# Kernel tuning notes

Hardware: AMD Instinct MI355X
Metric: run time of the kernel (lower is better)

Reference implementation:

```python
import jax, jax.numpy as jnp
import numpy as np

N, E = 50000, 800000
F_IN, H, OUT, L = 32, 128, 20, 4


def setup_inputs() -> dict:
    key = jax.random.key(0)
    ks = jax.random.split(key, 32)
    s = 0.05  # weight scale
    inp = {
        "h": jax.random.normal(ks[0], (N, F_IN), jnp.float32),
        "x": jax.random.normal(ks[1], (N, 3), jnp.float32),
        "edges": jax.random.randint(ks[2], (2, E), 0, N, jnp.int32),
        # embeddings
        "emb_in_w": jax.random.normal(ks[3], (F_IN, H)) * s,
        "emb_in_b": jnp.zeros((H,)),
        "emb_out_w": jax.random.normal(ks[4], (H, H)) * s,
        "emb_out_b": jnp.zeros((H,)),
        # per-layer stacked params
        "edge_w1": jax.random.normal(ks[5], (L, 2 * H + 1, H)) * s,
        "edge_b1": jnp.zeros((L, H)),
        "edge_w2": jax.random.normal(ks[6], (L, H, H)) * s,
        "edge_b2": jnp.zeros((L, H)),
        "att_w": jax.random.normal(ks[7], (L, H, 1)) * s,
        "att_b": jnp.zeros((L, 1)),
        "coord_w1": jax.random.normal(ks[8], (L, H, H)) * s,
        "coord_b1": jnp.zeros((L, H)),
        "coord_w2": jax.random.normal(ks[9], (L, H, 1)) * s,  # no bias (egnn_clean)
        "node_w1": jax.random.normal(ks[10], (L, 2 * H, H)) * s,
        "node_b1": jnp.zeros((L, H)),
        "node_w2": jax.random.normal(ks[11], (L, H, H)) * s,
        "node_b2": jnp.zeros((L, H)),
        # head MLP
        "head_w1": jax.random.normal(ks[12], (H, H)) * s,
        "head_b1": jnp.zeros((H,)),
        "head_w2": jax.random.normal(ks[13], (H, OUT)) * s,
        "head_b2": jnp.zeros((OUT,)),
    }
    return inp


def reference(h, x, edges, emb_in_w, emb_in_b, emb_out_w, emb_out_b,
              edge_w1, edge_b1, edge_w2, edge_b2, att_w, att_b,
              coord_w1, coord_b1, coord_w2,
              node_w1, node_b1, node_w2, node_b2,
              head_w1, head_b1, head_w2, head_b2):
    n = h.shape[0]
    row, col = edges[0], edges[1]
    h = h @ emb_in_w + emb_in_b
    for l in range(L):
        diff = x[row] - x[col]                       # [E,3]
        radial = jnp.sum(diff * diff, -1, keepdims=True)  # [E,1]
        m = jnp.concatenate([h[row], h[col], radial], -1)  # [E,2H+1]
        m = jax.nn.silu(m @ edge_w1[l] + edge_b1[l])
        m = jax.nn.silu(m @ edge_w2[l] + edge_b2[l])
        m = m * jax.nn.sigmoid(m @ att_w[l] + att_b[l])  # attention gate
        # coordinate update: segment mean of diff * coord_mlp(m)
        cw = jax.nn.silu(m @ coord_w1[l] + coord_b1[l]) @ coord_w2[l]  # [E,1]
        trans = diff * cw
        agg_x = jax.ops.segment_sum(trans, row, num_segments=n)
        cnt = jax.ops.segment_sum(jnp.ones((E, 1), trans.dtype), row, num_segments=n)
        x = x + agg_x / jnp.maximum(cnt, 1.0)
        # node update: residual MLP on [h, segment_sum(m)]
        agg_m = jax.ops.segment_sum(m, row, num_segments=n)
        hcat = jnp.concatenate([h, agg_m], -1)
        h = h + (jax.nn.silu(hcat @ node_w1[l] + node_b1[l]) @ node_w2[l] + node_b2[l])
    h = h @ emb_out_w + emb_out_b
    g = jnp.mean(h, axis=0)  # mean pool over nodes
    out = jax.nn.relu(g @ head_w1 + head_b1) @ head_w2 + head_b2
    return out[None, :]  # [1, OUT]
```

## Files before the change

### kernel.cpp

```cpp
#include <hip/hip_runtime.h>
#include <hip/hip_bf16.h>

#define NN   50000
#define EE   800000
#define FIN  32
#define HH   128
#define LL   4
#define NOUT 20

typedef __attribute__((ext_vector_type(8))) short bf16x8;
typedef __attribute__((ext_vector_type(4))) short short4v;
typedef __attribute__((ext_vector_type(4))) float f32x4;

__device__ __forceinline__ float silu_f(float v){ return v / (1.f + __expf(-v)); }
__device__ __forceinline__ float sigm_f(float v){ return 1.f / (1.f + __expf(-v)); }

__device__ __forceinline__ short f2bf(float v){
  union { float f; unsigned u; } a; a.f = v;
  unsigned r = a.u + 0x7fff + ((a.u >> 16) & 1);
  return (short)(r >> 16);
}
__device__ __forceinline__ float bf2f(short s){
  union { unsigned u; float f; } a; a.u = ((unsigned)(unsigned short)s) << 16;
  return a.f;
}

__device__ __forceinline__ f32x4 mfma16(bf16x8 a, bf16x8 b, f32x4 c){
  return __builtin_amdgcn_mfma_f32_16x16x32_bf16(a, b, c, 0, 0, 0);
}

__device__ __forceinline__ void gemm_mfma(const short* Ah, const short* Al,
                                          const short* __restrict__ Wh,
                                          const short* __restrict__ Wl,
                                          int lane, int wc0, f32x4 acc[4][2])
{
  const int cl = lane & 15, g = lane >> 4;
  const int wb0 = (wc0 + cl)*HH + g*8;
  const int wb1 = (wc0 + 16 + cl)*HH + g*8;
  #pragma unroll
  for (int kb = 0; kb < 4; kb++) {
    const int kk = kb*32 + g*8;
    bf16x8 bh[2], bl[2];
    bh[0] = *(const bf16x8*)&Wh[wb0 + kb*32];
    bl[0] = *(const bf16x8*)&Wl[wb0 + kb*32];
    bh[1] = *(const bf16x8*)&Wh[wb1 + kb*32];
    bl[1] = *(const bf16x8*)&Wl[wb1 + kb*32];
    #pragma unroll
    for (int fr = 0; fr < 4; fr++) {
      const int e = fr*16 + cl;
      const int off = e*128 + (kk ^ ((e&7)<<3));
      const bf16x8 ah = *(const bf16x8*)&Ah[off];
      const bf16x8 al = *(const bf16x8*)&Al[off];
      #pragma unroll
      for (int cf = 0; cf < 2; cf++) {
        acc[fr][cf] = mfma16(ah, bh[cf], acc[fr][cf]);
        acc[fr][cf] = mfma16(ah, bl[cf], acc[fr][cf]);
        acc[fr][cf] = mfma16(al, bh[cf], acc[fr][cf]);
      }
    }
  }
}

__device__ __forceinline__ void stage_p(const short* __restrict__ hbi,
                                        const short* __restrict__ hlo,
                                        const int* idx, short* Ah, short* Al, int tid)
{
  const int e = tid >> 2;
  const int q = tid & 3;
  const int base = idx[e]*HH;
  #pragma unroll
  for (int u = 0; u < 4; u++) {
    const int c = q*8 + u*32;
    const int o = e*128 + (c ^ ((e&7)<<3));
    *(bf16x8*)&Ah[o] = *(const bf16x8*)&hbi[base + c];
    *(bf16x8*)&Al[o] = *(const bf16x8*)&hlo[base + c];
  }
}

__global__ __launch_bounds__(256)
void k_prep(const float* __restrict__ ew1, const float* __restrict__ ew2,
            const float* __restrict__ cw1v, short* __restrict__ wph,
            short* __restrict__ wpl)
{
  const int b = blockIdx.x;
  const int l = b >> 2, m = b & 3;
  const float* src = (m==0) ? ew1 + (size_t)l*(2*HH+1)*HH
                   : (m==1) ? ew1 + (size_t)l*(2*HH+1)*HH + HH*HH
                   : (m==2) ? ew2 + (size_t)l*HH*HH
                            : cw1v + (size_t)l*HH*HH;
  short* dh = wph + (size_t)b*HH*HH;
  short* dl = wpl + (size_t)b*HH*HH;
  for (int idx = threadIdx.x; idx < HH*HH; idx += 256) {
    const int k = idx >> 7, c = idx & 127;
    const float v = src[idx];
    const short hh = f2bf(v);
    dh[c*HH + k] = hh;
    dl[c*HH + k] = f2bf(v - bf2f(hh));
  }
}

__global__ __launch_bounds__(256)
void k_embed(const float* __restrict__ hin, const float* __restrict__ xin,
             const float* __restrict__ W, const float* __restrict__ b,
             float* __restrict__ hout, float* __restrict__ xout,
             short* __restrict__ hbi, short* __restrict__ hlo)
{
  __shared__ float wl[FIN*HH];
  const int tid = threadIdx.x;
  for (int j = tid; j < FIN*HH; j += 256) wl[j] = W[j];
  __syncthreads();
  const int c  = tid & (HH-1);
  const int no = tid >> 7;
  const int v  = blockIdx.x * 2 + no;
  if (v < NN) {
    const float* hr = hin + (size_t)v * FIN;
    float acc = b[c];
    #pragma unroll
    for (int k = 0; k < FIN; k++) acc = fmaf(hr[k], wl[k*HH + c], acc);
    hout[(size_t)v*HH + c] = acc;
    const short hh = f2bf(acc);
    hbi[(size_t)v*HH + c] = hh;
    hlo[(size_t)v*HH + c] = f2bf(acc - bf2f(hh));
    if (c < 3) xout[v*3 + c] = xin[v*3 + c];
  }
}

__global__ __launch_bounds__(256)
void k_count(const int* __restrict__ row, int* __restrict__ deg)
{
  const int e = blockIdx.x * 256 + threadIdx.x;
  if (e < EE) atomicAdd(&deg[row[e]], 1);
}

__global__ __launch_bounds__(1024)
void k_scan(const int* __restrict__ deg, int* __restrict__ offs, int* __restrict__ cursor)
{
  __shared__ int part[1024];
  const int t = threadIdx.x;
  const int base = t * 49;
  int s = 0;
  for (int i = 0; i < 49; i++) { const int idx = base + i; s += (idx < NN) ? deg[idx] : 0; }
  part[t] = s;
  __syncthreads();
  if (t == 0) { int run = 0; for (int i = 0; i < 1024; i++) { const int v = part[i]; part[i] = run; run += v; } }
  __syncthreads();
  int run = part[t];
  for (int i = 0; i < 49; i++) {
    const int idx = base + i;
    if (idx < NN) { offs[idx] = run; cursor[idx] = run; run += deg[idx]; }
  }
  if (t == 1023) offs[NN] = EE;
}

__global__ __launch_bounds__(256)
void k_pos(const int* __restrict__ row, int* __restrict__ cursor, int* __restrict__ pos)
{
  const int e = blockIdx.x * 256 + threadIdx.x;
  if (e < EE) pos[e] = atomicAdd(&cursor[row[e]], 1);
}

template<bool SC>
__global__ __launch_bounds__(256)
void k_edge(const short* __restrict__ hbi, const short* __restrict__ hlo,
            const float* __restrict__ xbuf,
            const int* __restrict__ row, const int* __restrict__ col,
            const int* __restrict__ pos,
            const short* __restrict__ wph, const short* __restrict__ wpl, int lidx,
            const float* __restrict__ W1, const float* __restrict__ b1,
            const float* __restrict__ b2,
            const float* __restrict__ attw, const float* __restrict__ attb,
            const float* __restrict__ cb1, const float* __restrict__ cw2,
            float* __restrict__ mbuf, float* __restrict__ aggx)
{
  __shared__ short Ah[64*128];
  __shared__ short Al[64*128];
  __shared__ float red[4][64];
  __shared__ float scal[64];
  __shared__ int   rowb[64];
  __shared__ int   colb[64];
  __shared__ int   posb[64];
  __shared__ float diffb[64][3];
  __shared__ float radb[64];

  const int tid  = threadIdx.x;
  const int lane = tid & 63;
  const int wv   = tid >> 6;
  const int cl   = lane & 15;
  const int g    = lane >> 4;
  const int wc0  = wv * 32;
  const int col0 = wc0 + cl;
  const int col1 = wc0 + 16 + cl;
  const int eb   = blockIdx.x * 64;

  const short* W1a_h = wph + (size_t)(lidx*4+0)*HH*HH;
  const short* W1a_l = wpl + (size_t)(lidx*4+0)*HH*HH;
  const short* W1b_h = wph + (size_t)(lidx*4+1)*HH*HH;
  const short* W1b_l = wpl + (size_t)(lidx*4+1)*HH*HH;
  const short* W2_h  = wph + (size_t)(lidx*4+2)*HH*HH;
  const short* W2_l  = wpl + (size_t)(lidx*4+2)*HH*HH;
  const short* C1_h  = wph + (size_t)(lidx*4+3)*HH*HH;
  const short* C1_l  = wpl + (size_t)(lidx*4+3)*HH*HH;

  if (tid < 64) {
    const int r  = row[eb + tid];
    const int c2 = col[eb + tid];
    rowb[tid] = r; colb[tid] = c2;
    if (SC) posb[tid] = pos[eb + tid];
    const float dx = xbuf[r*3+0] - xbuf[c2*3+0];
    const float dy = xbuf[r*3+1] - xbuf[c2*3+1];
    const float dz = xbuf[r*3+2] - xbuf[c2*3+2];
    diffb[tid][0] = dx; diffb[tid][1] = dy; diffb[tid][2] = dz;
    radb[tid] = dx*dx + dy*dy + dz*dz;
  }
  __syncthreads();

  stage_p(hbi, hlo, rowb, Ah, Al, tid);
  __syncthreads();

  f32x4 acc[4][2];
  #pragma unroll
  for (int fr = 0; fr < 4; fr++) { acc[fr][0] = (f32x4){0,0,0,0}; acc[fr][1] = (f32x4){0,0,0,0}; }
  gemm_mfma(Ah, Al, W1a_h, W1a_l, lane, wc0, acc);
  __syncthreads();

  stage_p(hbi, hlo, colb, Ah, Al, tid);
  __syncthreads();

  gemm_mfma(Ah, Al, W1b_h, W1b_l, lane, wc0, acc);

  {
    const float w256a = W1[(size_t)(2*HH)*HH + col0];
    const float w256b = W1[(size_t)(2*HH)*HH + col1];
    const float bba = b1[col0], bbb = b1[col1];
    #pragma unroll
    for (int fr = 0; fr < 4; fr++) {
      #pragma unroll
      for (int j = 0; j < 4; j++) {
        const int r = fr*16 + g*4 + j;
        const float rr = radb[r];
        acc[fr][0][j] = silu_f(fmaf(rr, w256a, acc[fr][0][j]) + bba);
        acc[fr][1][j] = silu_f(fmaf(rr, w256b, acc[fr][1][j]) + bbb);
      }
    }
  }
  __syncthreads();

  #pragma unroll
  for (int fr = 0; fr < 4; fr++) {
    #pragma unroll
    for (int j = 0; j < 4; j++) {
      const int r = fr*16 + g*4 + j;
      const int sw = (r&7)<<3;
      const float v0 = acc[fr][0][j], v1 = acc[fr][1][j];
      const short h0 = f2bf(v0), h1 = f2bf(v1);
      Ah[r*128 + (col0 ^ sw)] = h0;  Al[r*128 + (col0 ^ sw)] = f2bf(v0 - bf2f(h0));
      Ah[r*128 + (col1 ^ sw)] = h1;  Al[r*128 + (col1 ^ sw)] = f2bf(v1 - bf2f(h1));
    }
  }
  __syncthreads();

  f32x4 m2[4][2];
  #pragma unroll
  for (int fr = 0; fr < 4; fr++) { m2[fr][0] = (f32x4){0,0,0,0}; m2[fr][1] = (f32x4){0,0,0,0}; }
  gemm_mfma(Ah, Al, W2_h, W2_l, lane, wc0, m2);
  {
    const float bba = b2[col0], bbb = b2[col1];
    #pragma unroll
    for (int fr = 0; fr < 4; fr++) {
      #pragma unroll
      for (int j = 0; j < 4; j++) {
        m2[fr][0][j] = silu_f(m2[fr][0][j] + bba);
        m2[fr][1][j] = silu_f(m2[fr][1][j] + bbb);
      }
    }
  }

  {
    const float awa = attw[col0], awb = attw[col1];
    #pragma unroll
    for (int fr = 0; fr < 4; fr++) {
      #pragma unroll
      for (int j = 0; j < 4; j++) {
        float p = fmaf(m2[fr][0][j], awa, m2[fr][1][j]*awb);
        p += __shfl_xor(p, 1); p += __shfl_xor(p, 2);
        p += __shfl_xor(p, 4); p += __shfl_xor(p, 8);
        if (cl == 0) red[wv][fr*16 + g*4 + j] = p;
      }
    }
  }
  __syncthreads();
  if (tid < 64)
    scal[tid] = sigm_f(red[0][tid] + red[1][tid] + red[2][tid] + red[3][tid] + attb[0]);
  __syncthreads();

  #pragma unroll
  for (int fr = 0; fr < 4; fr++) {
    #pragma unroll
    for (int j = 0; j < 4; j++) {
      const int r = fr*16 + g*4 + j;
      const float sc = scal[r];
      const float v0 = m2[fr][0][j]*sc, v1 = m2[fr][1][j]*sc;
      if (SC) {
        float* dst = &mbuf[(size_t)posb[r]*HH];
        dst[col0] = v0; dst[col1] = v1;
      } else {
        float* dst = &mbuf[(size_t)rowb[r]*HH];
        atomicAdd(&dst[col0], v0); atomicAdd(&dst[col1], v1);
      }
      const int sw = (r&7)<<3;
      const short h0 = f2bf(v0), h1 = f2bf(v1);
      Ah[r*128 + (col0 ^ sw)] = h0;  Al[r*128 + (col0 ^ sw)] = f2bf(v0 - bf2f(h0));
      Ah[r*128 + (col1 ^ sw)] = h1;  Al[r*128 + (col1 ^ sw)] = f2bf(v1 - bf2f(h1));
    }
  }
  __syncthreads();

  f32x4 a3[4][2];
  #pragma unroll
  for (int fr = 0; fr < 4; fr++) { a3[fr][0] = (f32x4){0,0,0,0}; a3[fr][1] = (f32x4){0,0,0,0}; }
  gemm_mfma(Ah, Al, C1_h, C1_l, lane, wc0, a3);
  {
    const float bba = cb1[col0], bbb = cb1[col1];
    const float c2a = cw2[col0], c2b = cw2[col1];
    #pragma unroll
    for (int fr = 0; fr < 4; fr++) {
      #pragma unroll
      for (int j = 0; j < 4; j++) {
        float p = fmaf(silu_f(a3[fr][0][j] + bba), c2a, silu_f(a3[fr][1][j] + bbb)*c2b);
        p += __shfl_xor(p, 1); p += __shfl_xor(p, 2);
        p += __shfl_xor(p, 4); p += __shfl_xor(p, 8);
        if (cl == 0) red[wv][fr*16 + g*4 + j] = p;
      }
    }
  }
  __syncthreads();

  if (tid < 64) {
    const float cwv = red[0][tid] + red[1][tid] + red[2][tid] + red[3][tid];
    const int r = rowb[tid];
    atomicAdd(&aggx[r*3+0], diffb[tid][0]*cwv);
    atomicAdd(&aggx[r*3+1], diffb[tid][1]*cwv);
    atomicAdd(&aggx[r*3+2], diffb[tid][2]*cwv);
  }
}

__device__ __forceinline__ void gemm_accum(const float (*buf)[132], const float* __restrict__ W,
                                           int c, int eo, float acc[32])
{
  for (int k0 = 0; k0 < HH; k0 += 4) {
    const float w0 = W[(k0+0)*HH + c];
    const float w1 = W[(k0+1)*HH + c];
    const float w2 = W[(k0+2)*HH + c];
    const float w3 = W[(k0+3)*HH + c];
    #pragma unroll
    for (int i = 0; i < 32; i++) {
      const float4 a = *(const float4*)&buf[eo*32+i][k0];
      acc[i] = fmaf(a.x, w0, fmaf(a.y, w1, fmaf(a.z, w2, fmaf(a.w, w3, acc[i]))));
    }
  }
}

template<bool SC>
__global__ __launch_bounds__(256, 2)
void k_node(float* __restrict__ hbuf, float* __restrict__ xbuf,
            const float* __restrict__ mbuf, const int* __restrict__ offs,
            const float* __restrict__ aggx,
            const float* __restrict__ W1, const float* __restrict__ b1,
            const float* __restrict__ W2, const float* __restrict__ b2,
            short* __restrict__ hbi, short* __restrict__ hlo)
{
  __shared__ float bufA[64][132];
  __shared__ float bufB[64][132];
  const int tid = threadIdx.x;
  const int c   = tid & (HH-1);
  const int no  = tid >> 7;
  const int nb  = blockIdx.x * 64;

  #pragma unroll
  for (int i = 0; i < 32; i++) {
    const int v = nb + no*32 + i;
    bufA[no*32+i][c] = (v < NN) ? hbuf[(size_t)v*HH + c] : 0.f;
  }
  __syncthreads();

  float acc[32];
  #pragma unroll
  for (int i = 0; i < 32; i++) acc[i] = 0.f;
  gemm_accum(bufA, W1, c, no, acc);
  __syncthreads();

  for (int i = 0; i < 32; i++) {
    const int v = nb + no*32 + i;
    float s = 0.f;
    if (v < NN) {
      if (SC) {
        const int beg = offs[v], end = offs[v+1];
        for (int j = beg; j < end; j++) s += mbuf[(size_t)j*HH + c];
      } else {
        s = mbuf[(size_t)v*HH + c];
      }
    }
    bufA[no*32+i][c] = s;
  }
  __syncthreads();
  gemm_accum(bufA, W1 + HH*HH, c, no, acc);
  {
    const float bb = b1[c];
    #pragma unroll
    for (int i = 0; i < 32; i++) bufB[no*32+i][c] = silu_f(acc[i] + bb);
  }
  __syncthreads();

  #pragma unroll
  for (int i = 0; i < 32; i++) acc[i] = 0.f;
  gemm_accum(bufB, W2, c, no, acc);
  {
    const float bb = b2[c];
    #pragma unroll
    for (int i = 0; i < 32; i++) {
      const int v = nb + no*32 + i;
      if (v < NN) {
        const float hn = hbuf[(size_t)v*HH + c] + acc[i] + bb;
        hbuf[(size_t)v*HH + c] = hn;
        const short hh = f2bf(hn);
        hbi[(size_t)v*HH + c] = hh;
        hlo[(size_t)v*HH + c] = f2bf(hn - bf2f(hh));
      }
    }
  }

  if (tid < 64) {
    const int v = nb + tid;
    if (v < NN) {
      const float ct = fmaxf((float)(offs[v+1] - offs[v]), 1.f);
      xbuf[v*3+0] += aggx[v*3+0] / ct;
      xbuf[v*3+1] += aggx[v*3+1] / ct;
      xbuf[v*3+2] += aggx[v*3+2] / ct;
    }
  }
}

__global__ __launch_bounds__(128)
void k_pool(const float* __restrict__ h, float* __restrict__ g)
{
  const int c  = threadIdx.x;
  const int v0 = blockIdx.x * 100;
  float s = 0.f;
  for (int v = v0; v < v0 + 100; ++v) s += h[(size_t)v*HH + c];
  atomicAdd(&g[c], s);
}

__global__ __launch_bounds__(128)
void k_head(const float* __restrict__ g,
            const float* __restrict__ eow, const float* __restrict__ eob,
            const float* __restrict__ hw1, const float* __restrict__ hb1,
            const float* __restrict__ hw2, const float* __restrict__ hb2,
            float* __restrict__ out)
{
  __shared__ float gm[HH], ho[HH], t1[HH];
  const int c = threadIdx.x;
  gm[c] = g[c] * (1.f / (float)NN);
  __syncthreads();
  float a = eob[c];
  for (int k = 0; k < HH; k++) a = fmaf(gm[k], eow[k*HH + c], a);
  ho[c] = a;
  __syncthreads();
  float t = hb1[c];
  for (int k = 0; k < HH; k++) t = fmaf(ho[k], hw1[k*HH + c], t);
  t1[c] = fmaxf(t, 0.f);
  __syncthreads();
  if (c < NOUT) {
    float o = hb2[c];
    for (int k = 0; k < HH; k++) o = fmaf(t1[k], hw2[k*NOUT + c], o);
    out[c] = o;
  }
}

extern "C" void kernel_launch(void* const* d_in, const int* in_sizes, int n_in,
                              void* d_out, int out_size, void* d_ws, size_t ws_size,
                              hipStream_t stream)
{
  const float* in_h  = (const float*)d_in[0];
  const float* in_x  = (const float*)d_in[1];
  const int*   edges = (const int*)  d_in[2];
  const float* eiw   = (const float*)d_in[3];
  const float* eib   = (const float*)d_in[4];
  const float* eow   = (const float*)d_in[5];
  const float* eob   = (const float*)d_in[6];
  const float* ew1   = (const float*)d_in[7];
  const float* eb1   = (const float*)d_in[8];
  const float* ew2   = (const float*)d_in[9];
  const float* eb2   = (const float*)d_in[10];
  const float* attw  = (const float*)d_in[11];
  const float* attb  = (const float*)d_in[12];
  const float* cw1   = (const float*)d_in[13];
  const float* cb1   = (const float*)d_in[14];
  const float* cw2   = (const float*)d_in[15];
  const float* nw1   = (const float*)d_in[16];
  const float* nb1   = (const float*)d_in[17];
  const float* nw2   = (const float*)d_in[18];
  const float* nb2   = (const float*)d_in[19];
  const float* hw1   = (const float*)d_in[20];
  const float* hb1   = (const float*)d_in[21];
  const float* hw2   = (const float*)d_in[22];
  const float* hb2   = (const float*)d_in[23];

  const int* row = edges;
  const int* col = edges + EE;

  char* p = (char*)d_ws;
  auto alloc = [&](size_t bytes) { char* r = p; p += (bytes + 255) & ~(size_t)255; return r; };
  float* h    = (float*)alloc((size_t)NN*HH*4);
  float* x    = (float*)alloc((size_t)NN*3*4);
  float* aggx = (float*)alloc((size_t)NN*3*4);
  float* g    = (float*)alloc(HH*4);
  int*   deg  = (int*)  alloc((size_t)NN*4);
  int*   offs = (int*)  alloc((size_t)(NN+1)*4);
  int*   curs = (int*)  alloc((size_t)NN*4);
  int*   pos  = (int*)  alloc((size_t)EE*4);
  short* hbi  = (short*)alloc((size_t)NN*HH*2);
  short* hlo  = (short*)alloc((size_t)NN*HH*2);
  short* wph  = (short*)alloc((size_t)16*HH*HH*2);
  short* wpl  = (short*)alloc((size_t)16*HH*HH*2);
  const size_t baseUsed = (size_t)(p - (char*)d_ws);
  const bool sc = (ws_size >= baseUsed + (size_t)EE*HH*4);
  float* mbuf = (float*)alloc(sc ? (size_t)EE*HH*4 : (size_t)NN*HH*4);

  k_prep<<<16, 256, 0, stream>>>(ew1, ew2, cw1, wph, wpl);
  k_embed<<<NN/2, 256, 0, stream>>>(in_h, in_x, eiw, eib, h, x, hbi, hlo);

  hipMemsetAsync(deg, 0, (size_t)NN*4, stream);
  k_count<<<(EE+255)/256, 256, 0, stream>>>(row, deg);
  k_scan<<<1, 1024, 0, stream>>>(deg, offs, curs);
  k_pos<<<(EE+255)/256, 256, 0, stream>>>(row, curs, pos);

  for (int l = 0; l < LL; l++) {
    hipMemsetAsync(aggx, 0, (size_t)NN*3*4, stream);
    if (!sc) hipMemsetAsync(mbuf, 0, (size_t)NN*HH*4, stream);
    if (sc) {
      k_edge<true><<<EE/64, 256, 0, stream>>>(hbi, hlo, x, row, col, pos,
          wph, wpl, l,
          ew1 + (size_t)l*(2*HH+1)*HH, eb1 + l*HH, eb2 + l*HH,
          attw + l*HH, attb + l, cb1 + l*HH, cw2 + l*HH,
          mbuf, aggx);
      k_node<true><<<(NN + 63)/64, 256, 0, stream>>>(h, x, mbuf, offs, aggx,
          nw1 + (size_t)l*(2*HH)*HH, nb1 + l*HH,
          nw2 + (size_t)l*HH*HH,     nb2 + l*HH, hbi, hlo);
    } else {
      k_edge<false><<<EE/64, 256, 0, stream>>>(hbi, hlo, x, row, col, pos,
          wph, wpl, l,
          ew1 + (size_t)l*(2*HH+1)*HH, eb1 + l*HH, eb2 + l*HH,
          attw + l*HH, attb + l, cb1 + l*HH, cw2 + l*HH,
          mbuf, aggx);
      k_node<false><<<(NN + 63)/64, 256, 0, stream>>>(h, x, mbuf, offs, aggx,
          nw1 + (size_t)l*(2*HH)*HH, nb1 + l*HH,
          nw2 + (size_t)l*HH*HH,     nb2 + l*HH, hbi, hlo);
    }
  }

  hipMemsetAsync(g, 0, HH*4, stream);
  k_pool<<<500, 128, 0, stream>>>(h, g);
  k_head<<<1, 128, 0, stream>>>(g, eow, eob, hw1, hb1, hw2, hb2, (float*)d_out);
}
```

Measured before the change: 4.250 ms.

## Enlarge edge tile to 128 edges with 8 waves each owning 16 columns

The edge kernel now processes 128 edges per block with 512 threads. Each of the 8 waves computes a 16-column slice across all 8 row fragments, where before each wave covered 32 columns over 4 fragments. The col-side gather of h is prefetched into registers while the first GEMM runs, which removes one global-load wait between the two halves of the first layer. Each weight fragment is now reused across twice as many edges, at the cost of double the LDS footprint (about 64KB for Ah/Al), which limits how many blocks fit per CU.

```diff
diff --git a/kernel.cpp b/kernel.cpp
--- a/kernel.cpp
+++ b/kernel.cpp
@@ -7,6 +7,8 @@
 #define HH   128
 #define LL   4
 #define NOUT 20
+#define EPB  128
+#define ETHR 512
 
 typedef __attribute__((ext_vector_type(8))) short bf16x8;
 typedef __attribute__((ext_vector_type(4))) short short4v;
@@ -29,51 +31,27 @@
   return __builtin_amdgcn_mfma_f32_16x16x32_bf16(a, b, c, 0, 0, 0);
 }
 
-__device__ __forceinline__ void gemm_mfma(const short* Ah, const short* Al,
-                                          const short* __restrict__ Wh,
-                                          const short* __restrict__ Wl,
-                                          int lane, int wc0, f32x4 acc[4][2])
-{
-  const int cl = lane & 15, g = lane >> 4;
-  const int wb0 = (wc0 + cl)*HH + g*8;
-  const int wb1 = (wc0 + 16 + cl)*HH + g*8;
+__device__ __forceinline__ void gemm8(const short* Ah, const short* Al,
+                                      const short* __restrict__ Wh,
+                                      const short* __restrict__ Wl,
+                                      int cl, int g, int wc0, f32x4 acc[8])
+{
+  const int wb = (wc0 + cl)*HH + g*8;
   #pragma unroll
   for (int kb = 0; kb < 4; kb++) {
     const int kk = kb*32 + g*8;
-    bf16x8 bh[2], bl[2];
-    bh[0] = *(const bf16x8*)&Wh[wb0 + kb*32];
-    bl[0] = *(const bf16x8*)&Wl[wb0 + kb*32];
-    bh[1] = *(const bf16x8*)&Wh[wb1 + kb*32];
-    bl[1] = *(const bf16x8*)&Wl[wb1 + kb*32];
-    #pragma unroll
-    for (int fr = 0; fr < 4; fr++) {
+    const bf16x8 bh = *(const bf16x8*)&Wh[wb + kb*32];
+    const bf16x8 bl = *(const bf16x8*)&Wl[wb + kb*32];
+    #pragma unroll
+    for (int fr = 0; fr < 8; fr++) {
       const int e = fr*16 + cl;
       const int off = e*128 + (kk ^ ((e&7)<<3));
       const bf16x8 ah = *(const bf16x8*)&Ah[off];
       const bf16x8 al = *(const bf16x8*)&Al[off];
-      #pragma unroll
-      for (int cf = 0; cf < 2; cf++) {
-        acc[fr][cf] = mfma16(ah, bh[cf], acc[fr][cf]);
-        acc[fr][cf] = mfma16(ah, bl[cf], acc[fr][cf]);
-        acc[fr][cf] = mfma16(al, bh[cf], acc[fr][cf]);
-      }
-    }
-  }
-}
-
-__device__ __forceinline__ void stage_p(const short* __restrict__ hbi,
-                                        const short* __restrict__ hlo,
-                                        const int* idx, short* Ah, short* Al, int tid)
-{
-  const int e = tid >> 2;
-  const int q = tid & 3;
-  const int base = idx[e]*HH;
-  #pragma unroll
-  for (int u = 0; u < 4; u++) {
-    const int c = q*8 + u*32;
-    const int o = e*128 + (c ^ ((e&7)<<3));
-    *(bf16x8*)&Ah[o] = *(const bf16x8*)&hbi[base + c];
-    *(bf16x8*)&Al[o] = *(const bf16x8*)&hlo[base + c];
+      acc[fr] = mfma16(ah, bh, acc[fr]);
+      acc[fr] = mfma16(ah, bl, acc[fr]);
+      acc[fr] = mfma16(al, bh, acc[fr]);
+    }
   }
 }
 
@@ -160,7 +138,7 @@
 }
 
 template<bool SC>
-__global__ __launch_bounds__(256)
+__global__ __launch_bounds__(ETHR, 4)
 void k_edge(const short* __restrict__ hbi, const short* __restrict__ hlo,
             const float* __restrict__ xbuf,
             const int* __restrict__ row, const int* __restrict__ col,
@@ -172,25 +150,24 @@
             const float* __restrict__ cb1, const float* __restrict__ cw2,
             float* __restrict__ mbuf, float* __restrict__ aggx)
 {
-  __shared__ short Ah[64*128];
-  __shared__ short Al[64*128];
-  __shared__ float red[4][64];
-  __shared__ float scal[64];
-  __shared__ int   rowb[64];
-  __shared__ int   colb[64];
-  __shared__ int   posb[64];
-  __shared__ float diffb[64][3];
-  __shared__ float radb[64];
+  __shared__ short Ah[EPB*128];
+  __shared__ short Al[EPB*128];
+  __shared__ float red[8][EPB];
+  __shared__ float scal[EPB];
+  __shared__ int   rowb[EPB];
+  __shared__ int   colb[EPB];
+  __shared__ int   posb[EPB];
+  __shared__ float diffb[EPB][3];
+  __shared__ float radb[EPB];
 
   const int tid  = threadIdx.x;
   const int lane = tid & 63;
   const int wv   = tid >> 6;
   const int cl   = lane & 15;
   const int g    = lane >> 4;
-  const int wc0  = wv * 32;
+  const int wc0  = wv * 16;
   const int col0 = wc0 + cl;
-  const int col1 = wc0 + 16 + cl;
-  const int eb   = blockIdx.x * 64;
+  const int eb   = blockIdx.x * EPB;
 
   const short* W1a_h = wph + (size_t)(lidx*4+0)*HH*HH;
   const short* W1a_l = wpl + (size_t)(lidx*4+0)*HH*HH;
@@ -201,7 +178,7 @@
   const short* C1_h  = wph + (size_t)(lidx*4+3)*HH*HH;
   const short* C1_l  = wpl + (size_t)(lidx*4+3)*HH*HH;
 
-  if (tid < 64) {
+  if (tid < EPB) {
     const int r  = row[eb + tid];
     const int c2 = col[eb + tid];
     rowb[tid] = r; colb[tid] = c2;
@@ -214,74 +191,89 @@
   }
   __syncthreads();
 
-  stage_p(hbi, hlo, rowb, Ah, Al, tid);
-  __syncthreads();
-
-  f32x4 acc[4][2];
-  #pragma unroll
-  for (int fr = 0; fr < 4; fr++) { acc[fr][0] = (f32x4){0,0,0,0}; acc[fr][1] = (f32x4){0,0,0,0}; }
-  gemm_mfma(Ah, Al, W1a_h, W1a_l, lane, wc0, acc);
-  __syncthreads();
-
-  stage_p(hbi, hlo, colb, Ah, Al, tid);
-  __syncthreads();
-
-  gemm_mfma(Ah, Al, W1b_h, W1b_l, lane, wc0, acc);
-
-  {
-    const float w256a = W1[(size_t)(2*HH)*HH + col0];
-    const float w256b = W1[(size_t)(2*HH)*HH + col1];
-    const float bba = b1[col0], bbb = b1[col1];
-    #pragma unroll
-    for (int fr = 0; fr < 4; fr++) {
+  const int se = tid >> 2;
+  const int sq = tid & 3;
+  {
+    const int base = rowb[se]*HH;
+    #pragma unroll
+    for (int u = 0; u < 4; u++) {
+      const int c = sq*8 + u*32;
+      const int o = se*128 + (c ^ ((se&7)<<3));
+      *(bf16x8*)&Ah[o] = *(const bf16x8*)&hbi[base + c];
+      *(bf16x8*)&Al[o] = *(const bf16x8*)&hlo[base + c];
+    }
+  }
+  bf16x8 pch[4], pcl[4];
+  {
+    const int base = colb[se]*HH;
+    #pragma unroll
+    for (int u = 0; u < 4; u++) {
+      const int c = sq*8 + u*32;
+      pch[u] = *(const bf16x8*)&hbi[base + c];
+      pcl[u] = *(const bf16x8*)&hlo[base + c];
+    }
+  }
+  __syncthreads();
+
+  f32x4 acc[8];
+  #pragma unroll
+  for (int fr = 0; fr < 8; fr++) acc[fr] = (f32x4){0,0,0,0};
+  gemm8(Ah, Al, W1a_h, W1a_l, cl, g, wc0, acc);
+  __syncthreads();
+
+  {
+    #pragma unroll
+    for (int u = 0; u < 4; u++) {
+      const int c = sq*8 + u*32;
+      const int o = se*128 + (c ^ ((se&7)<<3));
+      *(bf16x8*)&Ah[o] = pch[u];
+      *(bf16x8*)&Al[o] = pcl[u];
+    }
+  }
+  __syncthreads();
+
+  gemm8(Ah, Al, W1b_h, W1b_l, cl, g, wc0, acc);
+  {
+    const float w256 = W1[(size_t)(2*HH)*HH + col0];
+    const float bb   = b1[col0];
+    #pragma unroll
+    for (int fr = 0; fr < 8; fr++) {
       #pragma unroll
       for (int j = 0; j < 4; j++) {
         const int r = fr*16 + g*4 + j;
-        const float rr = radb[r];
-        acc[fr][0][j] = silu_f(fmaf(rr, w256a, acc[fr][0][j]) + bba);
-        acc[fr][1][j] = silu_f(fmaf(rr, w256b, acc[fr][1][j]) + bbb);
+        acc[fr][j] = silu_f(fmaf(radb[r], w256, acc[fr][j]) + bb);
       }
     }
   }
   __syncthreads();
 
   #pragma unroll
-  for (int fr = 0; fr < 4; fr++) {
+  for (int fr = 0; fr < 8; fr++) {
     #pragma unroll
     for (int j = 0; j < 4; j++) {
       const int r = fr*16 + g*4 + j;
       const int sw = (r&7)<<3;
-      const float v0 = acc[fr][0][j], v1 = acc[fr][1][j];
-      const short h0 = f2bf(v0), h1 = f2bf(v1);
-      Ah[r*128 + (col0 ^ sw)] = h0;  Al[r*128 + (col0 ^ sw)] = f2bf(v0 - bf2f(h0));
-      Ah[r*128 + (col1 ^ sw)] = h1;  Al[r*128 + (col1 ^ sw)] = f2bf(v1 - bf2f(h1));
-    }
-  }
-  __syncthreads();
-
-  f32x4 m2[4][2];
-  #pragma unroll
-  for (int fr = 0; fr < 4; fr++) { m2[fr][0] = (f32x4){0,0,0,0}; m2[fr][1] = (f32x4){0,0,0,0}; }
-  gemm_mfma(Ah, Al, W2_h, W2_l, lane, wc0, m2);
-  {
-    const float bba = b2[col0], bbb = b2[col1];
-    #pragma unroll
-    for (int fr = 0; fr < 4; fr++) {
+      const float v = acc[fr][j];
+      const short h0 = f2bf(v);
+      Ah[r*128 + (col0 ^ sw)] = h0;
+      Al[r*128 + (col0 ^ sw)] = f2bf(v - bf2f(h0));
+    }
+  }
+  __syncthreads();
+
+  f32x4 m2[8];
+  #pragma unroll
+  for (int fr = 0; fr < 8; fr++) m2[fr] = (f32x4){0,0,0,0};
+  gemm8(Ah, Al, W2_h, W2_l, cl, g, wc0, m2);
+  {
+    const float bb = b2[col0];
+    const float aw = attw[col0];
+    #pragma unroll
+    for (int fr = 0; fr < 8; fr++) {
       #pragma unroll
       for (int j = 0; j < 4; j++) {
-        m2[fr][0][j] = silu_f(m2[fr][0][j] + bba);
-        m2[fr][1][j] = silu_f(m2[fr][1][j] + bbb);
-      }
-    }
-  }
-
-  {
-    const float awa = attw[col0], awb = attw[col1];
-    #pragma unroll
-    for (int fr = 0; fr < 4; fr++) {
-      #pragma unroll
-      for (int j = 0; j < 4; j++) {
-        float p = fmaf(m2[fr][0][j], awa, m2[fr][1][j]*awb);
+        m2[fr][j] = silu_f(m2[fr][j] + bb);
+        float p = m2[fr][j] * aw;
         p += __shfl_xor(p, 1); p += __shfl_xor(p, 2);
         p += __shfl_xor(p, 4); p += __shfl_xor(p, 8);
         if (cl == 0) red[wv][fr*16 + g*4 + j] = p;
@@ -289,44 +281,46 @@
     }
   }
   __syncthreads();
-  if (tid < 64)
-    scal[tid] = sigm_f(red[0][tid] + red[1][tid] + red[2][tid] + red[3][tid] + attb[0]);
-  __syncthreads();
-
-  #pragma unroll
-  for (int fr = 0; fr < 4; fr++) {
+
+  if (tid < EPB) {
+    float s = attb[0];
+    #pragma unroll
+    for (int w = 0; w < 8; w++) s += red[w][tid];
+    scal[tid] = sigm_f(s);
+  }
+  __syncthreads();
+
+  #pragma unroll
+  for (int fr = 0; fr < 8; fr++) {
     #pragma unroll
     for (int j = 0; j < 4; j++) {
       const int r = fr*16 + g*4 + j;
-      const float sc = scal[r];
-      const float v0 = m2[fr][0][j]*sc, v1 = m2[fr][1][j]*sc;
+      const float v = m2[fr][j] * scal[r];
       if (SC) {
-        float* dst = &mbuf[(size_t)posb[r]*HH];
-        dst[col0] = v0; dst[col1] = v1;
+        mbuf[(size_t)posb[r]*HH + col0] = v;
       } else {
-        float* dst = &mbuf[(size_t)rowb[r]*HH];
-        atomicAdd(&dst[col0], v0); atomicAdd(&dst[col1], v1);
+        atomicAdd(&mbuf[(size_t)rowb[r]*HH + col0], v);
       }
       const int sw = (r&7)<<3;
-      const short h0 = f2bf(v0), h1 = f2bf(v1);
-      Ah[r*128 + (col0 ^ sw)] = h0;  Al[r*128 + (col0 ^ sw)] = f2bf(v0 - bf2f(h0));
-      Ah[r*128 + (col1 ^ sw)] = h1;  Al[r*128 + (col1 ^ sw)] = f2bf(v1 - bf2f(h1));
-    }
-  }
-  __syncthreads();
-
-  f32x4 a3[4][2];
-  #pragma unroll
-  for (int fr = 0; fr < 4; fr++) { a3[fr][0] = (f32x4){0,0,0,0}; a3[fr][1] = (f32x4){0,0,0,0}; }
-  gemm_mfma(Ah, Al, C1_h, C1_l, lane, wc0, a3);
-  {
-    const float bba = cb1[col0], bbb = cb1[col1];
-    const float c2a = cw2[col0], c2b = cw2[col1];
-    #pragma unroll
-    for (int fr = 0; fr < 4; fr++) {
+      const short h0 = f2bf(v);
+      Ah[r*128 + (col0 ^ sw)] = h0;
+      Al[r*128 + (col0 ^ sw)] = f2bf(v - bf2f(h0));
+    }
+  }
+  __syncthreads();
+
+  f32x4 a3[8];
+  #pragma unroll
+  for (int fr = 0; fr < 8; fr++) a3[fr] = (f32x4){0,0,0,0};
+  gemm8(Ah, Al, C1_h, C1_l, cl, g, wc0, a3);
+  {
+    const float bb = cb1[col0];
+    const float c2 = cw2[col0];
+    #pragma unroll
+    for (int fr = 0; fr < 8; fr++) {
       #pragma unroll
       for (int j = 0; j < 4; j++) {
-        float p = fmaf(silu_f(a3[fr][0][j] + bba), c2a, silu_f(a3[fr][1][j] + bbb)*c2b);
+        float p = silu_f(a3[fr][j] + bb) * c2;
         p += __shfl_xor(p, 1); p += __shfl_xor(p, 2);
         p += __shfl_xor(p, 4); p += __shfl_xor(p, 8);
         if (cl == 0) red[wv][fr*16 + g*4 + j] = p;
@@ -335,8 +329,10 @@
   }
   __syncthreads();
 
-  if (tid < 64) {
-    const float cwv = red[0][tid] + red[1][tid] + red[2][tid] + red[3][tid];
+  if (tid < EPB) {
+    float cwv = 0.f;
+    #pragma unroll
+    for (int w = 0; w < 8; w++) cwv += red[w][tid];
     const int r = rowb[tid];
     atomicAdd(&aggx[r*3+0], diffb[tid][0]*cwv);
     atomicAdd(&aggx[r*3+1], diffb[tid][1]*cwv);
@@ -538,7 +534,7 @@
     hipMemsetAsync(aggx, 0, (size_t)NN*3*4, stream);
     if (!sc) hipMemsetAsync(mbuf, 0, (size_t)NN*HH*4, stream);
     if (sc) {
-      k_edge<true><<<EE/64, 256, 0, stream>>>(hbi, hlo, x, row, col, pos,
+      k_edge<true><<<EE/EPB, ETHR, 0, stream>>>(hbi, hlo, x, row, col, pos,
           wph, wpl, l,
           ew1 + (size_t)l*(2*HH+1)*HH, eb1 + l*HH, eb2 + l*HH,
           attw + l*HH, attb + l, cb1 + l*HH, cw2 + l*HH,
@@ -547,7 +543,7 @@
           nw1 + (size_t)l*(2*HH)*HH, nb1 + l*HH,
           nw2 + (size_t)l*HH*HH,     nb2 + l*HH, hbi, hlo);
     } else {
-      k_edge<false><<<EE/64, 256, 0, stream>>>(hbi, hlo, x, row, col, pos,
+      k_edge<false><<<EE/EPB, ETHR, 0, stream>>>(hbi, hlo, x, row, col, pos,
           wph, wpl, l,
           ew1 + (size_t)l*(2*HH+1)*HH, eb1 + l*HH, eb2 + l*HH,
           attw + l*HH, attb + l, cb1 + l*HH, cw2 + l*HH,
```

New measurement: 3.771 ms. 1.13x faster.
